# Kernel optimization log

Hardware: AMD Instinct MI355X
Metric: run time of the kernel (lower is better)

## Reference

```python
import jax, jax.numpy as jnp
import numpy as np

D_MODEL = 2048
NUM_Q_HEADS = 16
NUM_KV_HEADS = 4
HEAD_DIM = D_MODEL // NUM_Q_HEADS  # 128
NUM_GROUPS = NUM_Q_HEADS // NUM_KV_HEADS  # 4
ROPE_BASE = 10000.0


def _rope_cos_sin(seq_len, head_dim):
    inv_freq = 1.0 / (ROPE_BASE ** (jnp.arange(0, head_dim, 2, dtype=jnp.float32) / head_dim))
    t = jnp.arange(seq_len, dtype=jnp.float32)
    freqs = jnp.outer(t, inv_freq)            # [S, head_dim/2]
    emb = jnp.concatenate([freqs, freqs], -1)  # [S, head_dim]
    return jnp.cos(emb)[None, :, None, :], jnp.sin(emb)[None, :, None, :]


def _rotate_half(x):
    half = x.shape[-1] // 2
    return jnp.concatenate([-x[..., half:], x[..., :half]], axis=-1)


def setup_inputs() -> dict:
    key = jax.random.key(0)
    k0, k1, k2, k3, k4 = jax.random.split(key, 5)
    B, S = 2, 2048
    kv_dim = HEAD_DIM * NUM_KV_HEADS
    scale = D_MODEL ** -0.5
    return {
        "x": jax.random.normal(k0, (B, S, D_MODEL), jnp.float32),
        "attention_mask": jnp.ones((B, S), jnp.int32),
        "Wq": jax.random.normal(k1, (D_MODEL, D_MODEL), jnp.float32) * scale,
        "Wk": jax.random.normal(k2, (D_MODEL, kv_dim), jnp.float32) * scale,
        "Wv": jax.random.normal(k3, (D_MODEL, kv_dim), jnp.float32) * scale,
        "Wo": jax.random.normal(k4, (D_MODEL, D_MODEL), jnp.float32) * scale,
    }


def reference(x, attention_mask, Wq, Wk, Wv, Wo):
    B, S, _ = x.shape
    q = (x @ Wq).reshape(B, S, NUM_Q_HEADS, HEAD_DIM)
    k = (x @ Wk).reshape(B, S, NUM_KV_HEADS, HEAD_DIM)
    v = (x @ Wv).reshape(B, S, NUM_KV_HEADS, HEAD_DIM)

    cos, sin = _rope_cos_sin(S, HEAD_DIM)  # [1,S,1,hd]
    q = q * cos + _rotate_half(q) * sin
    k = k * cos + _rotate_half(k) * sin

    # [B, H, S, hd]; replicate KV heads across groups (repeat_interleave)
    q = q.transpose(0, 2, 1, 3)
    k = jnp.repeat(k.transpose(0, 2, 1, 3), NUM_GROUPS, axis=1)
    v = jnp.repeat(v.transpose(0, 2, 1, 3), NUM_GROUPS, axis=1)

    scale = HEAD_DIM ** -0.5
    scores = jnp.einsum("bhqd,bhkd->bhqk", q, k) * scale
    mask = attention_mask[:, None, None, :]  # [B,1,1,S] over keys
    scores = jnp.where(mask == 0, jnp.float32(-jnp.inf), scores)
    probs = jax.nn.softmax(scores, axis=-1)
    out = jnp.einsum("bhqk,bhkd->bhqd", probs, v)
    out = out.transpose(0, 2, 1, 3).reshape(B, S, D_MODEL)
    return out @ Wo
```

## Files before the change

### kernel.cpp

```cpp
#include <hip/hip_runtime.h>
#include <hip/hip_bf16.h>

typedef __attribute__((ext_vector_type(4))) float f32x4;
typedef __attribute__((ext_vector_type(16))) float f32x16;
typedef __attribute__((ext_vector_type(8))) short s16x8;
typedef __attribute__((ext_vector_type(4))) short s16x4;
typedef __attribute__((ext_vector_type(2))) unsigned int u32x2;

__device__ __forceinline__ float fexp2(float x) {
    float y; asm("v_exp_f32 %0, %1" : "=v"(y) : "v"(x)); return y;
}

__global__ void rope_tables(float* __restrict__ cosT, float* __restrict__ sinT) {
    const int s = blockIdx.x, j = threadIdx.x;
    const float inv = exp2f(-(float)j * (13.287712379549449f / 64.f));
    const float f = (float)s * inv;
    cosT[s * 64 + j] = cosf(f);
    sinT[s * 64 + j] = sinf(f);
}

__global__ void mask_bias(const int* __restrict__ mask, float* __restrict__ mb, int n) {
    const int i = blockIdx.x * 256 + threadIdx.x;
    if (i < n) mb[i] = (mask[i] == 0) ? -1e30f : 0.f;
}

__global__ __launch_bounds__(256)
void cast_f32_bf16(const float* __restrict__ src, __hip_bfloat16* __restrict__ dst, int n4) {
    const int i = blockIdx.x * 256 + threadIdx.x;
    if (i < n4) {
        f32x4 v = *reinterpret_cast<const f32x4*>(src + (size_t)i * 4);
        union { s16x4 v4; __hip_bfloat16 h[4]; } u;
#pragma unroll
        for (int j = 0; j < 4; ++j) u.h[j] = __float2bfloat16(v[j]);
        *reinterpret_cast<s16x4*>(dst + (size_t)i * 4) = u.v4;
    }
}

__global__ __launch_bounds__(256)
void transpose_cast_all(const float* __restrict__ Wq, const float* __restrict__ Wk,
                        const float* __restrict__ Wv, const float* __restrict__ Wo,
                        __hip_bfloat16* __restrict__ wqkv_t, __hip_bfloat16* __restrict__ wo_t) {
    __shared__ __align__(16) float t[32][33];
    const int tx = threadIdx.x, ty = threadIdx.y;
    const int xseg = blockIdx.x;
    const int r0 = blockIdx.y * 32;
    const float* src; __hip_bfloat16* dst; int C, c0;
    if (xseg < 64)      { src = Wq; dst = wqkv_t;                  C = 2048; c0 = xseg * 32; }
    else if (xseg < 80) { src = Wk; dst = wqkv_t + 2048ULL * 2048; C = 512;  c0 = (xseg - 64) * 32; }
    else if (xseg < 96) { src = Wv; dst = wqkv_t + 2560ULL * 2048; C = 512;  c0 = (xseg - 80) * 32; }
    else                { src = Wo; dst = wo_t;                    C = 2048; c0 = (xseg - 96) * 32; }
#pragma unroll
    for (int i = 0; i < 32; i += 8)
        t[ty + i][tx] = src[(size_t)(r0 + ty + i) * C + c0 + tx];
    __syncthreads();
#pragma unroll
    for (int i = 0; i < 32; i += 8)
        dst[(size_t)(c0 + ty + i) * 2048 + r0 + tx] = __float2bfloat16(t[tx][ty + i]);
}

__global__ __launch_bounds__(256)
void vt_transpose(const __hip_bfloat16* __restrict__ qkv, __hip_bfloat16* __restrict__ Vt) {
    __shared__ unsigned short t[32][33];
    const int tx = threadIdx.x, ty = threadIdx.y;
    const int s0 = blockIdx.x * 32, d0 = blockIdx.y * 32;
    const int bh = blockIdx.z, b = bh >> 2, hh = bh & 3;
    const unsigned short* q = (const unsigned short*)qkv;
#pragma unroll
    for (int i = 0; i < 32; i += 8)
        t[ty + i][tx] = q[(size_t)(b * 2048 + s0 + ty + i) * 3072 + 2560 + hh * 128 + d0 + tx];
    __syncthreads();
#pragma unroll
    for (int i = 0; i < 32; i += 8)
        ((unsigned short*)Vt)[((size_t)(bh * 128) + d0 + ty + i) * 2048 + s0 + tx] = t[tx][ty + i];
}

template<int NI, bool BF16OUT>
__global__ __launch_bounds__(512, 1)
void gemm256_bt(const __hip_bfloat16* __restrict__ A,
                const __hip_bfloat16* __restrict__ Bt,
                void* __restrict__ Cv, int M, int N, int K, int NX) {
    __shared__ __align__(16) __hip_bfloat16 sm[4][2][8192];
    const int tid = threadIdx.x;
    const int l = tid & 63, w = tid >> 6;
    const int lo = l & 15, hi = l >> 4;
    const int wm = w >> 2, wn = w & 3;
    const int id = blockIdx.x, slot = id >> 3;
    const int by = (id & 7) * 2 + slot / NX;
    const int bx = slot % NX;
    const int row0 = by * 256;
    const int col0 = bx * (NI * 64);
    const int nk = K >> 5;

    f32x4 acc[8][NI];
#pragma unroll
    for (int mi = 0; mi < 8; ++mi)
#pragma unroll
        for (int ni = 0; ni < NI; ++ni) acc[mi][ni] = f32x4{0.f, 0.f, 0.f, 0.f};

    auto ldlds = [&](const __hip_bfloat16* gsrc, __hip_bfloat16* ldst) {
        __builtin_amdgcn_global_load_lds(
            (const __attribute__((address_space(1))) void*)gsrc,
            (__attribute__((address_space(3))) void*)ldst, 16, 0, 0);
    };
    auto stage = [&](int kt) {
        const int s = kt & 3, k0 = kt << 5;
#pragma unroll
        for (int i = 0; i < 2; ++i) {
            const int c = i * 512 + tid;
            const int r = c >> 2, sw = ((c & 3) ^ ((r >> 1) & 3)) * 8;
            ldlds(A + (size_t)(row0 + r) * K + k0 + sw, &sm[s][0][c * 8]);
        }
        {
            const int c = tid;
            const int r = c >> 2, sw = ((c & 3) ^ ((r >> 1) & 3)) * 8;
            ldlds(Bt + (size_t)(col0 + r) * K + k0 + sw, &sm[s][1][c * 8]);
        }
        if constexpr (NI == 4) {
            const int c = 512 + tid;
            const int r = c >> 2, sw = ((c & 3) ^ ((r >> 1) & 3)) * 8;
            ldlds(Bt + (size_t)(col0 + r) * K + k0 + sw, &sm[s][1][c * 8]);
        } else if constexpr (NI == 3) {
            if (tid < 256) {
                const int c = 512 + tid;
                const int r = c >> 2, sw = ((c & 3) ^ ((r >> 1) & 3)) * 8;
                ldlds(Bt + (size_t)(col0 + r) * K + k0 + sw, &sm[s][1][c * 8]);
            }
        }
    };

    stage(0); stage(1); stage(2);
    for (int kt = 0; kt < nk; ++kt) {
        const int s = kt & 3;
        if (kt < nk - 2) {
            if constexpr (NI == 4)      asm volatile("s_waitcnt vmcnt(8)" ::: "memory");
            else if constexpr (NI == 2) asm volatile("s_waitcnt vmcnt(6)" ::: "memory");
            else { if (tid < 256) asm volatile("s_waitcnt vmcnt(8)" ::: "memory");
                   else           asm volatile("s_waitcnt vmcnt(6)" ::: "memory"); }
        } else if (kt == nk - 2) {
            if constexpr (NI == 4)      asm volatile("s_waitcnt vmcnt(4)" ::: "memory");
            else if constexpr (NI == 2) asm volatile("s_waitcnt vmcnt(3)" ::: "memory");
            else { if (tid < 256) asm volatile("s_waitcnt vmcnt(4)" ::: "memory");
                   else           asm volatile("s_waitcnt vmcnt(3)" ::: "memory"); }
        } else {
            asm volatile("s_waitcnt vmcnt(0)" ::: "memory");
        }
        asm volatile("s_waitcnt lgkmcnt(0)" ::: "memory");
        asm volatile("s_barrier" ::: "memory");
        if (kt + 3 < nk) stage(kt + 3);

        s16x8 af[8], bf[NI];
        const int rsw = ((lo >> 1) & 3);
#pragma unroll
        for (int mi = 0; mi < 8; ++mi)
            af[mi] = *reinterpret_cast<const s16x8*>(
                &sm[s][0][(wm * 128 + mi * 16 + lo) * 32 + ((hi ^ rsw) * 8)]);
#pragma unroll
        for (int ni = 0; ni < NI; ++ni)
            bf[ni] = *reinterpret_cast<const s16x8*>(
                &sm[s][1][(wn * NI * 16 + ni * 16 + lo) * 32 + ((hi ^ rsw) * 8)]);
        __builtin_amdgcn_s_setprio(1);
#pragma unroll
        for (int mi = 0; mi < 8; ++mi)
#pragma unroll
            for (int ni = 0; ni < NI; ++ni)
                acc[mi][ni] = __builtin_amdgcn_mfma_f32_16x16x32_bf16(af[mi], bf[ni], acc[mi][ni], 0, 0, 0);
        __builtin_amdgcn_s_setprio(0);
    }
    const int rbase = row0 + wm * 128 + hi * 4;
    const int cbase = col0 + wn * NI * 16 + lo;
    if constexpr (BF16OUT) {
        __hip_bfloat16* C = (__hip_bfloat16*)Cv;
#pragma unroll
        for (int mi = 0; mi < 8; ++mi)
#pragma unroll
            for (int ni = 0; ni < NI; ++ni)
#pragma unroll
                for (int r = 0; r < 4; ++r)
                    C[(size_t)(rbase + mi * 16 + r) * N + cbase + ni * 16] =
                        __float2bfloat16(acc[mi][ni][r]);
    } else {
        float* C = (float*)Cv;
#pragma unroll
        for (int mi = 0; mi < 8; ++mi)
#pragma unroll
            for (int ni = 0; ni < NI; ++ni)
#pragma unroll
                for (int r = 0; r < 4; ++r)
                    C[(size_t)(rbase + mi * 16 + r) * N + cbase + ni * 16] = acc[mi][ni][r];
    }
}

__global__ __launch_bounds__(256)
void rope_scatter(const __hip_bfloat16* __restrict__ qkv,
                  const float* __restrict__ cosT, const float* __restrict__ sinT,
                  __hip_bfloat16* __restrict__ Qr, __hip_bfloat16* __restrict__ Kr) {
    const int m = blockIdx.y;
    const int col4 = blockIdx.x * 256 + threadIdx.x;
    if (col4 >= 640) return;
    const int col = col4 * 4;
    const int b = m >> 11, s = m & 2047;
    const int d = col & 127;
    const int j = d & 63;
    union { s16x4 v4; __hip_bfloat16 h[4]; } vv, pp, u;
    vv.v4 = *reinterpret_cast<const s16x4*>(qkv + (size_t)m * 3072 + col);
    pp.v4 = *reinterpret_cast<const s16x4*>(qkv + (size_t)m * 3072 + (col ^ 64));
    const f32x4 c4 = *reinterpret_cast<const f32x4*>(cosT + s * 64 + j);
    const f32x4 s4 = *reinterpret_cast<const f32x4*>(sinT + s * 64 + j);
    const float sgn = (d < 64) ? -1.f : 1.f;
#pragma unroll
    for (int i = 0; i < 4; ++i)
        u.h[i] = __float2bfloat16(__bfloat162float(vv.h[i]) * c4[i] +
                                  sgn * __bfloat162float(pp.h[i]) * s4[i]);
    if (col < 2048) {
        const int hh = col >> 7;
        *reinterpret_cast<s16x4*>(&Qr[((size_t)(b * 16 + hh) * 2048 + s) * 128 + d]) = u.v4;
    } else {
        const int hh = (col - 2048) >> 7;
        *reinterpret_cast<s16x4*>(&Kr[((size_t)(b * 4 + hh) * 2048 + s) * 128 + d]) = u.v4;
    }
}

__global__ __launch_bounds__(256, 2)
void attn_kernel(const __hip_bfloat16* __restrict__ Qr,
                 const __hip_bfloat16* __restrict__ Kr,
                 const __hip_bfloat16* __restrict__ Vt,
                 const float* __restrict__ maskb,
                 __hip_bfloat16* __restrict__ Oo) {
    const int S = 2048;
    const int id = blockIdx.x;
    const int v = (id & 7) * 64 + (id >> 3);
    const int qt = v & 15;
    const int bh = v >> 4;
    const int b = bh >> 4, h = bh & 15, kvh = h >> 2;
    const int tid = threadIdx.x;
    const int l = tid & 63, wv_ = tid >> 6;
    const int lq = l & 31, hi2 = l >> 5;
    __shared__ __align__(16) __hip_bfloat16 Ks[2][64 * 128];
    __shared__ __align__(16) __hip_bfloat16 Vs[2][128 * 64];

    const __hip_bfloat16* Qb = Qr + (size_t)(b * 16 + h) * S * 128;
    const __hip_bfloat16* Kb = Kr + (size_t)(b * 4 + kvh) * S * 128;
    const __hip_bfloat16* Vb = Vt + (size_t)(b * 4 + kvh) * 128 * S;
    const float* mrow = maskb + b * S;

    const int qrow = qt * 128 + wv_ * 32 + lq;
    s16x8 qf[8];
#pragma unroll
    for (int ks = 0; ks < 8; ++ks)
        qf[ks] = *reinterpret_cast<const s16x8*>(Qb + (size_t)qrow * 128 + ks * 16 + hi2 * 8);

    float m_run = 0.f, l_run = 0.f;
    f32x16 o[4];
#pragma unroll
    for (int dt = 0; dt < 4; ++dt)
#pragma unroll
        for (int r = 0; r < 16; ++r) o[dt][r] = 0.f;
    const float scale2 = 0.12751682f;

    const int krow = tid >> 4, kc8 = tid & 15;
    const int koff = (kc8 ^ (krow & 7)) * 8;
    const int vrow = tid >> 3, vc8 = tid & 7;
    const int voff = (vc8 ^ (vrow & 7)) * 8;

    s16x8 kreg[4], vreg[4];
    auto load_tile = [&](int kv0) {
#pragma unroll
        for (int i = 0; i < 4; ++i)
            kreg[i] = *reinterpret_cast<const s16x8*>(
                Kb + (size_t)(kv0 + i * 16 + krow) * 128 + kc8 * 8);
#pragma unroll
        for (int i = 0; i < 4; ++i)
            vreg[i] = *reinterpret_cast<const s16x8*>(
                Vb + (size_t)(i * 32 + vrow) * S + kv0 + vc8 * 8);
    };

    auto body = [&](int kt, __hip_bfloat16* Kc, __hip_bfloat16* Vc) {
        const int kv0 = kt * 64;
        f32x4 bi[2][4];
#pragma unroll
        for (int sub = 0; sub < 2; ++sub)
#pragma unroll
            for (int r4 = 0; r4 < 4; ++r4)
                bi[sub][r4] = *reinterpret_cast<const f32x4*>(
                    mrow + kv0 + sub * 32 + r4 * 8 + hi2 * 4);
#pragma unroll
        for (int i = 0; i < 4; ++i)
            *reinterpret_cast<s16x8*>(Kc + (i * 16 + krow) * 128 + koff) = kreg[i];
#pragma unroll
        for (int i = 0; i < 4; ++i)
            *reinterpret_cast<s16x8*>(Vc + (i * 32 + vrow) * 64 + voff) = vreg[i];
        if (kt < 31) load_tile(kv0 + 64);
        asm volatile("s_waitcnt lgkmcnt(0)" ::: "memory");
        asm volatile("s_barrier" ::: "memory");

        f32x16 sc[2];
#pragma unroll
        for (int sub = 0; sub < 2; ++sub)
#pragma unroll
            for (int r = 0; r < 16; ++r) sc[sub][r] = 0.f;
        __builtin_amdgcn_s_setprio(1);
#pragma unroll
        for (int sub = 0; sub < 2; ++sub) {
            const int kr = sub * 32 + lq;
            const int ksw = kr & 7;
#pragma unroll
            for (int ks = 0; ks < 8; ++ks) {
                s16x8 kf = *reinterpret_cast<const s16x8*>(
                    Kc + kr * 128 + (((ks * 2 + hi2) ^ ksw) * 8));
                sc[sub] = __builtin_amdgcn_mfma_f32_32x32x16_bf16(kf, qf[ks], sc[sub], 0, 0, 0);
            }
        }
        __builtin_amdgcn_s_setprio(0);
#pragma unroll
        for (int sub = 0; sub < 2; ++sub)
#pragma unroll
            for (int r = 0; r < 16; ++r)
                sc[sub][r] = fmaf(sc[sub][r], scale2, bi[sub][r >> 2][r & 3]);
        float mx = sc[0][0];
#pragma unroll
        for (int sub = 0; sub < 2; ++sub)
#pragma unroll
            for (int r = 0; r < 16; ++r) mx = fmaxf(mx, sc[sub][r]);
        float ss = 0.f;
#pragma unroll
        for (int sub = 0; sub < 2; ++sub)
#pragma unroll
            for (int r = 0; r < 16; ++r) {
                sc[sub][r] = fexp2(sc[sub][r] - m_run);
                ss += sc[sub][r];
            }
        mx = fmaxf(mx, __shfl_xor(mx, 32));
        if (__ballot(mx > m_run + 11.5417f) != 0ull) {
            const float mnew = fmaxf(m_run, mx);
            const float alpha = fexp2(m_run - mnew);
            m_run = mnew;
            l_run *= alpha;
            ss *= alpha;
#pragma unroll
            for (int sub = 0; sub < 2; ++sub)
#pragma unroll
                for (int r = 0; r < 16; ++r) sc[sub][r] *= alpha;
#pragma unroll
            for (int dt = 0; dt < 4; ++dt)
#pragma unroll
                for (int r = 0; r < 16; ++r) o[dt][r] *= alpha;
        }
        ss += __shfl_xor(ss, 32);
        l_run += ss;
        unsigned int wvp[8][2];
#pragma unroll
        for (int g = 0; g < 8; ++g) {
            const int sub = g >> 2, r4 = g & 3;
            asm("v_cvt_pk_bf16_f32 %0, %1, %2"
                : "=v"(wvp[g][0]) : "v"(sc[sub][r4 * 4 + 0]), "v"(sc[sub][r4 * 4 + 1]));
            asm("v_cvt_pk_bf16_f32 %0, %1, %2"
                : "=v"(wvp[g][1]) : "v"(sc[sub][r4 * 4 + 2]), "v"(sc[sub][r4 * 4 + 3]));
        }
        __builtin_amdgcn_s_setprio(1);
#pragma unroll
        for (int ks = 0; ks < 4; ++ks) {
            u32x2 r0 = __builtin_amdgcn_permlane32_swap(wvp[2 * ks][0], wvp[2 * ks + 1][0], false, false);
            u32x2 r1 = __builtin_amdgcn_permlane32_swap(wvp[2 * ks][1], wvp[2 * ks + 1][1], false, false);
            union { unsigned int u[4]; s16x8 v; } pf;
            pf.u[0] = r0.x; pf.u[1] = r1.x; pf.u[2] = r0.y; pf.u[3] = r1.y;
#pragma unroll
            for (int dt = 0; dt < 4; ++dt) {
                const int dvr = dt * 32 + lq;
                s16x8 vf = *reinterpret_cast<const s16x8*>(
                    Vc + dvr * 64 + (((ks * 2 + hi2) ^ (dvr & 7)) * 8));
                o[dt] = __builtin_amdgcn_mfma_f32_32x32x16_bf16(vf, pf.v, o[dt], 0, 0, 0);
            }
        }
        __builtin_amdgcn_s_setprio(0);
    };

    load_tile(0);
    for (int kt2 = 0; kt2 < 16; ++kt2) {
        body(2 * kt2,     &Ks[0][0], &Vs[0][0]);
        body(2 * kt2 + 1, &Ks[1][0], &Vs[1][0]);
    }
    const float inv = 1.f / l_run;
    const size_t obase = (size_t)(b * S + qt * 128 + wv_ * 32 + lq) * 2048 + h * 128;
#pragma unroll
    for (int dt = 0; dt < 4; ++dt)
#pragma unroll
        for (int r4 = 0; r4 < 4; ++r4) {
            union { s16x4 v4; __hip_bfloat16 hh[4]; } u;
#pragma unroll
            for (int j = 0; j < 4; ++j)
                u.hh[j] = __float2bfloat16(o[dt][r4 * 4 + j] * inv);
            *reinterpret_cast<s16x4*>(&Oo[obase + dt * 32 + r4 * 8 + hi2 * 4]) = u.v4;
        }
}

extern "C" void kernel_launch(void* const* d_in, const int* in_sizes, int n_in,
                              void* d_out, int out_size, void* d_ws, size_t ws_size,
                              hipStream_t stream) {
    const float* x  = (const float*)d_in[0];
    const int* mask = (const int*)d_in[1];
    const float* Wq = (const float*)d_in[2];
    const float* Wk = (const float*)d_in[3];
    const float* Wv = (const float*)d_in[4];
    const float* Wo = (const float*)d_in[5];
    float* out = (float*)d_out;

    char* ws = (char*)d_ws;
    size_t off = 0;
    auto alloc = [&](size_t bytes) -> void* {
        void* p = ws + off;
        off += (bytes + 255) & ~(size_t)255;
        return p;
    };
    __hip_bfloat16* xb     = (__hip_bfloat16*)alloc(4096ULL * 2048 * 2);
    __hip_bfloat16* wqkv_t = (__hip_bfloat16*)alloc(3072ULL * 2048 * 2);
    __hip_bfloat16* wo_t   = (__hip_bfloat16*)alloc(2048ULL * 2048 * 2);
    __hip_bfloat16* qkvb   = (__hip_bfloat16*)alloc(4096ULL * 3072 * 2);
    __hip_bfloat16* Kr     = (__hip_bfloat16*)alloc(2ULL * 4 * 2048 * 128 * 2);
    __hip_bfloat16* Vt     = (__hip_bfloat16*)alloc(2ULL * 4 * 2048 * 128 * 2);
    float*          cosT   = (float*)alloc(2048ULL * 64 * 4);
    float*          sinT   = (float*)alloc(2048ULL * 64 * 4);
    float*          maskb  = (float*)alloc(2ULL * 2048 * 4);
    __hip_bfloat16* attno  = (__hip_bfloat16*)alloc(4096ULL * 2048 * 2);
    __hip_bfloat16* Qr    = xb;

    rope_tables<<<dim3(2048), dim3(64), 0, stream>>>(cosT, sinT);
    mask_bias<<<dim3(16), dim3(256), 0, stream>>>(mask, maskb, 4096);
    cast_f32_bf16<<<dim3(8192), dim3(256), 0, stream>>>(x, xb, 2097152);
    transpose_cast_all<<<dim3(160, 64), dim3(32, 8), 0, stream>>>(Wq, Wk, Wv, Wo, wqkv_t, wo_t);

    gemm256_bt<3, true><<<dim3(256), dim3(512), 0, stream>>>(xb, wqkv_t, qkvb, 4096, 3072, 2048, 16);
    rope_scatter<<<dim3(3, 4096), dim3(256), 0, stream>>>(qkvb, cosT, sinT, Qr, Kr);
    vt_transpose<<<dim3(64, 4, 8), dim3(32, 8), 0, stream>>>(qkvb, Vt);
    attn_kernel<<<dim3(512), dim3(256), 0, stream>>>(Qr, Kr, Vt, maskb, attno);
    gemm256_bt<2, false><<<dim3(256), dim3(512), 0, stream>>>(attno, wo_t, out, 4096, 2048, 2048, 16);
}
```

Measured before the change: 218.4 us.

## Add pipelined 128x256 output-projection GEMM and merge rope/mask prep kernels

Replaces the output projection GEMM with a new 128x256-tile kernel. It uses a 4-stage direct global-to-LDS load pipeline with XOR swizzling, explicit waitcnt control and MFMA priority hints, aiming to hide memory latency better. It also merges the rope table and mask bias kernels into one launch to cut launch overhead. The new GEMM relies on a hand-managed vmcnt sequence and a fixed block mapping tied to these shapes.

```diff
diff --git a/kernel.cpp b/kernel.cpp
--- a/kernel.cpp
+++ b/kernel.cpp
@@ -11,17 +11,21 @@
     float y; asm("v_exp_f32 %0, %1" : "=v"(y) : "v"(x)); return y;
 }
 
-__global__ void rope_tables(float* __restrict__ cosT, float* __restrict__ sinT) {
-    const int s = blockIdx.x, j = threadIdx.x;
-    const float inv = exp2f(-(float)j * (13.287712379549449f / 64.f));
-    const float f = (float)s * inv;
-    cosT[s * 64 + j] = cosf(f);
-    sinT[s * 64 + j] = sinf(f);
-}
-
-__global__ void mask_bias(const int* __restrict__ mask, float* __restrict__ mb, int n) {
-    const int i = blockIdx.x * 256 + threadIdx.x;
-    if (i < n) mb[i] = (mask[i] == 0) ? -1e30f : 0.f;
+__global__ void tables_prep(float* __restrict__ cosT, float* __restrict__ sinT,
+                            const int* __restrict__ mask, float* __restrict__ mb) {
+    const int bid = blockIdx.x;
+    if (bid < 2048) {
+        const int s = bid, j = threadIdx.x;
+        const float inv = exp2f(-(float)j * (13.287712379549449f / 64.f));
+        const float f = (float)s * inv;
+        cosT[s * 64 + j] = cosf(f);
+        sinT[s * 64 + j] = sinf(f);
+    } else {
+        const int base = (bid - 2048) * 64 + threadIdx.x;
+#pragma unroll
+        for (int k = 0; k < 4; ++k)
+            mb[base + k * 1024] = (mask[base + k * 1024] == 0) ? -1e30f : 0.f;
+    }
 }
 
 __global__ __launch_bounds__(256)
@@ -188,6 +192,88 @@
                 for (int r = 0; r < 4; ++r)
                     C[(size_t)(rbase + mi * 16 + r) * N + cbase + ni * 16] = acc[mi][ni][r];
     }
+}
+
+__global__ __launch_bounds__(512, 1)
+void gemm128x256_bt(const __hip_bfloat16* __restrict__ A,
+                    const __hip_bfloat16* __restrict__ Bt,
+                    float* __restrict__ C, int M, int N, int K) {
+    __shared__ __align__(16) __hip_bfloat16 smA[4][4096];
+    __shared__ __align__(16) __hip_bfloat16 smB[4][8192];
+    const int tid = threadIdx.x;
+    const int l = tid & 63, w = tid >> 6;
+    const int lo = l & 15, hi = l >> 4;
+    const int wm = w >> 2, wn = w & 3;
+    const int id = blockIdx.x, slot = id >> 3;
+    const int by = (id & 7) * 4 + slot / 8;
+    const int bx = slot % 8;
+    const int row0 = by * 128;
+    const int col0 = bx * 256;
+    const int nk = K >> 5;
+
+    f32x4 acc[4][4];
+#pragma unroll
+    for (int mi = 0; mi < 4; ++mi)
+#pragma unroll
+        for (int ni = 0; ni < 4; ++ni) acc[mi][ni] = f32x4{0.f, 0.f, 0.f, 0.f};
+
+    auto ldlds = [&](const __hip_bfloat16* gsrc, __hip_bfloat16* ldst) {
+        __builtin_amdgcn_global_load_lds(
+            (const __attribute__((address_space(1))) void*)gsrc,
+            (__attribute__((address_space(3))) void*)ldst, 16, 0, 0);
+    };
+    auto stage = [&](int kt) {
+        const int s = kt & 3, k0 = kt << 5;
+        {
+            const int c = tid;
+            const int r = c >> 2, sw = ((c & 3) ^ ((r >> 1) & 3)) * 8;
+            ldlds(A + (size_t)(row0 + r) * K + k0 + sw, &smA[s][c * 8]);
+        }
+#pragma unroll
+        for (int i = 0; i < 2; ++i) {
+            const int c = i * 512 + tid;
+            const int r = c >> 2, sw = ((c & 3) ^ ((r >> 1) & 3)) * 8;
+            ldlds(Bt + (size_t)(col0 + r) * K + k0 + sw, &smB[s][c * 8]);
+        }
+    };
+
+    stage(0); stage(1); stage(2);
+    for (int kt = 0; kt < nk; ++kt) {
+        const int s = kt & 3;
+        if (kt < nk - 2)       asm volatile("s_waitcnt vmcnt(6)" ::: "memory");
+        else if (kt == nk - 2) asm volatile("s_waitcnt vmcnt(3)" ::: "memory");
+        else                   asm volatile("s_waitcnt vmcnt(0)" ::: "memory");
+        asm volatile("s_waitcnt lgkmcnt(0)" ::: "memory");
+        asm volatile("s_barrier" ::: "memory");
+        if (kt + 3 < nk) stage(kt + 3);
+
+        s16x8 af[4], bf[4];
+        const int rsw = ((lo >> 1) & 3);
+#pragma unroll
+        for (int mi = 0; mi < 4; ++mi)
+            af[mi] = *reinterpret_cast<const s16x8*>(
+                &smA[s][(wm * 64 + mi * 16 + lo) * 32 + ((hi ^ rsw) * 8)]);
+#pragma unroll
+        for (int ni = 0; ni < 4; ++ni)
+            bf[ni] = *reinterpret_cast<const s16x8*>(
+                &smB[s][(wn * 64 + ni * 16 + lo) * 32 + ((hi ^ rsw) * 8)]);
+        __builtin_amdgcn_s_setprio(1);
+#pragma unroll
+        for (int mi = 0; mi < 4; ++mi)
+#pragma unroll
+            for (int ni = 0; ni < 4; ++ni)
+                acc[mi][ni] = __builtin_amdgcn_mfma_f32_16x16x32_bf16(af[mi], bf[ni], acc[mi][ni], 0, 0, 0);
+        __builtin_amdgcn_s_setprio(0);
+    }
+    const int rbase = row0 + wm * 64 + hi * 4;
+    const int cbase = col0 + wn * 64 + lo;
+#pragma unroll
+    for (int mi = 0; mi < 4; ++mi)
+#pragma unroll
+        for (int ni = 0; ni < 4; ++ni)
+#pragma unroll
+            for (int r = 0; r < 4; ++r)
+                C[(size_t)(rbase + mi * 16 + r) * N + cbase + ni * 16] = acc[mi][ni][r];
 }
 
 __global__ __launch_bounds__(256)
@@ -423,8 +509,7 @@
     __hip_bfloat16* attno  = (__hip_bfloat16*)alloc(4096ULL * 2048 * 2);
     __hip_bfloat16* Qr    = xb;
 
-    rope_tables<<<dim3(2048), dim3(64), 0, stream>>>(cosT, sinT);
-    mask_bias<<<dim3(16), dim3(256), 0, stream>>>(mask, maskb, 4096);
+    tables_prep<<<dim3(2064), dim3(64), 0, stream>>>(cosT, sinT, mask, maskb);
     cast_f32_bf16<<<dim3(8192), dim3(256), 0, stream>>>(x, xb, 2097152);
     transpose_cast_all<<<dim3(160, 64), dim3(32, 8), 0, stream>>>(Wq, Wk, Wv, Wo, wqkv_t, wo_t);
 
@@ -432,5 +517,5 @@
     rope_scatter<<<dim3(3, 4096), dim3(256), 0, stream>>>(qkvb, cosT, sinT, Qr, Kr);
     vt_transpose<<<dim3(64, 4, 8), dim3(32, 8), 0, stream>>>(qkvb, Vt);
     attn_kernel<<<dim3(512), dim3(256), 0, stream>>>(Qr, Kr, Vt, maskb, attno);
-    gemm256_bt<2, false><<<dim3(256), dim3(512), 0, stream>>>(attno, wo_t, out, 4096, 2048, 2048, 16);
-}
+    gemm128x256_bt<<<dim3(256), dim3(512), 0, stream>>>(attno, wo_t, out, 4096, 2048, 2048);
+}
```

After: 231.1 us. 1.06x slower.
